# Kernel tuning notes

Measured on AMD Instinct MI355X. Metric: run time of the kernel, lower is better.

Reference implementation:

```python
import jax, jax.numpy as jnp
import numpy as np

D_MODEL = 512
NUM_HEADS = 8
HEAD_DIM = D_MODEL // NUM_HEADS
EPS = 1e-6


def setup_inputs() -> dict:
    key = jax.random.key(0)
    ks = jax.random.split(key, 9)
    s = 1.0 / np.sqrt(D_MODEL)
    x = jax.random.normal(ks[0], (4, 8192, D_MODEL), dtype=jnp.float32)
    Wq = jax.random.uniform(ks[1], (D_MODEL, D_MODEL), jnp.float32, -s, s)
    bq = jax.random.uniform(ks[2], (D_MODEL,), jnp.float32, -s, s)
    Wk = jax.random.uniform(ks[3], (D_MODEL, D_MODEL), jnp.float32, -s, s)
    bk = jax.random.uniform(ks[4], (D_MODEL,), jnp.float32, -s, s)
    Wv = jax.random.uniform(ks[5], (D_MODEL, D_MODEL), jnp.float32, -s, s)
    bv = jax.random.uniform(ks[6], (D_MODEL,), jnp.float32, -s, s)
    Wo = jax.random.uniform(ks[7], (D_MODEL, D_MODEL), jnp.float32, -s, s)
    bo = jax.random.uniform(ks[8], (D_MODEL,), jnp.float32, -s, s)
    return {"x": x, "Wq": Wq, "bq": bq, "Wk": Wk, "bk": bk,
            "Wv": Wv, "bv": bv, "Wo": Wo, "bo": bo}


def _feature_map(t):
    # ELU(x) + 1
    return jax.nn.elu(t) + 1.0


def reference(x, Wq, bq, Wk, bk, Wv, bv, Wo, bo):
    B, N, C = x.shape
    H, D = NUM_HEADS, HEAD_DIM
    # projections: torch Linear computes x @ W.T + b
    q = (x @ Wq.T + bq).reshape(B, N, H, D).transpose(0, 2, 1, 3)  # [B,H,N,D]
    k = (x @ Wk.T + bk).reshape(B, N, H, D).transpose(0, 2, 1, 3)
    v = (x @ Wv.T + bv).reshape(B, N, H, D).transpose(0, 2, 1, 3)
    q = _feature_map(q)
    k = _feature_map(k)
    # kv: [B,H,D,D] = k^T v   (global, non-causal linear attention)
    kv = jnp.einsum('bhnd,bhne->bhde', k, v)
    # normalizer: q . sum_n(k)  -> [B,H,N,1]
    k_sum = k.sum(axis=2)  # [B,H,D]
    z = jnp.einsum('bhnd,bhd->bhn', q, k_sum)[..., None] + EPS
    out = jnp.einsum('bhnd,bhde->bhne', q, kv) / z  # [B,H,N,D]
    out = out.transpose(0, 2, 1, 3).reshape(B, N, C)
    return out @ Wo.T + bo
```

## Files before the change

kernel.cpp:

```cpp
#include <hip/hip_runtime.h>
#include <hip/hip_bf16.h>

typedef __attribute__((ext_vector_type(8))) short short8;
typedef __attribute__((ext_vector_type(4))) float f32x4;
typedef unsigned short u16;
typedef unsigned int u32;

#define T_TOK 32768
#define CDIM  512
#define HEADS 8
#define HD    64
#define NSEQ  8192

#define AS1 __attribute__((address_space(1)))
#define AS3 __attribute__((address_space(3)))

__device__ __forceinline__ u16 f2bf(float f) {
  u32 u = __builtin_bit_cast(u32, f);
  u = u + 0x7fffu + ((u >> 16) & 1u);
  return (u16)(u >> 16);
}
__device__ __forceinline__ float bf2f(u16 s) {
  return __builtin_bit_cast(float, ((u32)s) << 16);
}

__global__ __launch_bounds__(256) void k_convx(const float* __restrict__ x,
                                               u16* __restrict__ xb) {
  size_t i = (size_t)blockIdx.x * 256 + threadIdx.x;
  size_t stride = (size_t)gridDim.x * 256;
  size_t total = (size_t)T_TOK * 512 / 8;
  for (; i < total; i += stride) {
    float4 a = *reinterpret_cast<const float4*>(&x[i * 8]);
    float4 b = *reinterpret_cast<const float4*>(&x[i * 8 + 4]);
    ushort4 r0, r1;
    r0.x = f2bf(a.x); r0.y = f2bf(a.y); r0.z = f2bf(a.z); r0.w = f2bf(a.w);
    r1.x = f2bf(b.x); r1.y = f2bf(b.y); r1.z = f2bf(b.z); r1.w = f2bf(b.w);
    *reinterpret_cast<ushort4*>(&xb[i * 8])     = r0;
    *reinterpret_cast<ushort4*>(&xb[i * 8 + 4]) = r1;
  }
}

__global__ void k_pack_w(const float* __restrict__ Wq, const float* __restrict__ Wk,
                         const float* __restrict__ Wv, const float* __restrict__ Wo,
                         u16* __restrict__ Wcat) {
  int idx = blockIdx.x * 256 + threadIdx.x;
  int c = idx & 511;
  int o2 = idx >> 9;
  const float* W = (o2 < 512) ? Wq : (o2 < 1024) ? Wk : (o2 < 1536) ? Wv : Wo;
  int o = o2 & 511;
  Wcat[idx] = f2bf(W[o * 512 + c]);
}

__global__ __launch_bounds__(256, 2) void k_gemm0(const u16* __restrict__ Ag,
    const u16* __restrict__ Wcat,
    const float* __restrict__ b0, const float* __restrict__ b1, const float* __restrict__ b2,
    u16* __restrict__ qkv) {
  constexpr int NT = 6;
  __shared__ u16 As[128][64];
  __shared__ u16 Bs[256][64];
  int bid = blockIdx.x;
  constexpr int GRID = (T_TOK / 128) * NT;
  constexpr int CHUNK = GRID / 8;
  int swz = (bid & 7) * CHUNK + (bid >> 3);
  int m0 = (swz / NT) * 128;
  int n0 = (swz % NT) * 256;
  int tid = threadIdx.x;
  int lane = tid & 63, w = tid >> 6;
  int wr = w >> 1, wc = w & 1;
  f32x4 acc_a[4][4], acc_b[4][4];
  _Pragma("unroll")
  for (int i = 0; i < 4; ++i)
    _Pragma("unroll")
    for (int j = 0; j < 4; ++j) { acc_a[i][j] = (f32x4)0.0f; acc_b[i][j] = (f32x4)0.0f; }

  int grl = lane >> 3;
  int gcl = (((lane & 7) ^ grl)) * 8;
  int l15 = lane & 15, lhi = lane >> 4, sx = lane & 7;

  for (int t = 0; t < 8; ++t) {
    int k0 = t * 64;
    _Pragma("unroll")
    for (int i = 0; i < 4; ++i) {
      int r = w * 32 + i * 8;
      __builtin_amdgcn_global_load_lds(
          (const AS1 void*)&Ag[(size_t)(m0 + r + grl) * 512 + k0 + gcl],
          (AS3 void*)&As[r][0], 16, 0, 0);
    }
    _Pragma("unroll")
    for (int i = 0; i < 8; ++i) {
      int r = w * 64 + i * 8;
      __builtin_amdgcn_global_load_lds(
          (const AS1 void*)&Wcat[(size_t)(n0 + r + grl) * 512 + k0 + gcl],
          (AS3 void*)&Bs[r][0], 16, 0, 0);
    }
    __syncthreads();
    _Pragma("unroll")
    for (int kk = 0; kk < 2; ++kk) {
      int slot = (kk * 4 + lhi) ^ sx;
      short8 af[4], bfa[4], bfb[4];
      _Pragma("unroll")
      for (int m = 0; m < 4; ++m)
        af[m] = *reinterpret_cast<const short8*>(&As[wr * 64 + m * 16 + l15][slot * 8]);
      _Pragma("unroll")
      for (int n = 0; n < 4; ++n)
        bfa[n] = *reinterpret_cast<const short8*>(&Bs[wc * 128 + n * 16 + l15][slot * 8]);
      _Pragma("unroll")
      for (int n = 0; n < 4; ++n)
        bfb[n] = *reinterpret_cast<const short8*>(&Bs[wc * 128 + 64 + n * 16 + l15][slot * 8]);
      _Pragma("unroll")
      for (int m = 0; m < 4; ++m)
        _Pragma("unroll")
        for (int n = 0; n < 4; ++n)
          acc_a[m][n] = __builtin_amdgcn_mfma_f32_16x16x32_bf16(af[m], bfa[n], acc_a[m][n], 0, 0, 0);
      _Pragma("unroll")
      for (int m = 0; m < 4; ++m)
        _Pragma("unroll")
        for (int n = 0; n < 4; ++n)
          acc_b[m][n] = __builtin_amdgcn_mfma_f32_16x16x32_bf16(af[m], bfb[n], acc_b[m][n], 0, 0, 0);
    }
    __syncthreads();
  }

  _Pragma("unroll")
  for (int m = 0; m < 4; ++m) {
    int row = m0 + wr * 64 + m * 16 + lhi * 4;
    _Pragma("unroll")
    for (int nh = 0; nh < 2; ++nh) {
      _Pragma("unroll")
      for (int n = 0; n < 4; ++n) {
        int col = n0 + wc * 128 + nh * 64 + n * 16 + l15;
        float bias = (col < 512) ? b0[col] : (col < 1024) ? b1[col - 512] : b2[col - 1024];
        _Pragma("unroll")
        for (int j = 0; j < 4; ++j) {
          float vv = (nh == 0 ? acc_a[m][n][j] : acc_b[m][n][j]) + bias;
          if (col < 1024) vv = (vv > 0.0f) ? (vv + 1.0f) : __expf(vv);
          qkv[(size_t)(row + j) * 1536 + col] = f2bf(vv);
        }
      }
    }
  }
}

__global__ __launch_bounds__(256, 4) void k_gemm1(const u16* __restrict__ Ag,
    const u16* __restrict__ Wcat, const float* __restrict__ b0,
    float* __restrict__ out) {
  constexpr int NT = 4;
  __shared__ u16 As[128][64];
  __shared__ u16 Bs[128][64];
  int bid = blockIdx.x;
  constexpr int GRID = (T_TOK / 128) * NT;
  constexpr int CHUNK = GRID / 8;
  int swz = (bid & 7) * CHUNK + (bid >> 3);
  int m0 = (swz / NT) * 128;
  int n0 = (swz % NT) * 128;
  int tid = threadIdx.x;
  int lane = tid & 63, w = tid >> 6;
  int wr = w >> 1, wc = w & 1;
  f32x4 acc[4][4];
  _Pragma("unroll")
  for (int i = 0; i < 4; ++i)
    _Pragma("unroll")
    for (int j = 0; j < 4; ++j) acc[i][j] = (f32x4)0.0f;

  const u16* Bg = Wcat + (size_t)1536 * 512;
  int grl = lane >> 3;
  int gcl = (((lane & 7) ^ grl)) * 8;
  int l15 = lane & 15, lhi = lane >> 4, sx = lane & 7;

  for (int t = 0; t < 8; ++t) {
    int k0 = t * 64;
    _Pragma("unroll")
    for (int i = 0; i < 4; ++i) {
      int r = w * 32 + i * 8;
      __builtin_amdgcn_global_load_lds(
          (const AS1 void*)&Ag[(size_t)(m0 + r + grl) * 512 + k0 + gcl],
          (AS3 void*)&As[r][0], 16, 0, 0);
      __builtin_amdgcn_global_load_lds(
          (const AS1 void*)&Bg[(size_t)(n0 + r + grl) * 512 + k0 + gcl],
          (AS3 void*)&Bs[r][0], 16, 0, 0);
    }
    __syncthreads();
    _Pragma("unroll")
    for (int kk = 0; kk < 2; ++kk) {
      int slot = (kk * 4 + lhi) ^ sx;
      short8 af[4], bfr[4];
      _Pragma("unroll")
      for (int m = 0; m < 4; ++m)
        af[m] = *reinterpret_cast<const short8*>(&As[wr * 64 + m * 16 + l15][slot * 8]);
      _Pragma("unroll")
      for (int n = 0; n < 4; ++n)
        bfr[n] = *reinterpret_cast<const short8*>(&Bs[wc * 64 + n * 16 + l15][slot * 8]);
      _Pragma("unroll")
      for (int m = 0; m < 4; ++m)
        _Pragma("unroll")
        for (int n = 0; n < 4; ++n)
          acc[m][n] = __builtin_amdgcn_mfma_f32_16x16x32_bf16(af[m], bfr[n], acc[m][n], 0, 0, 0);
    }
    __syncthreads();
  }

  _Pragma("unroll")
  for (int m = 0; m < 4; ++m) {
    int row = m0 + wr * 64 + m * 16 + lhi * 4;
    _Pragma("unroll")
    for (int n = 0; n < 4; ++n) {
      int col = n0 + wc * 64 + n * 16 + l15;
      float bias = b0[col];
      _Pragma("unroll")
      for (int j = 0; j < 4; ++j)
        out[(size_t)(row + j) * 512 + col] = acc[m][n][j] + bias;
    }
  }
}

__global__ __launch_bounds__(256) void k_kvstats(const u16* __restrict__ qkv,
    float* __restrict__ kvp, float* __restrict__ ksp) {
  __shared__ u16 kt[64][32];
  __shared__ u16 vt[64][32];
  __shared__ float ks_red[4][64];
  int hh = blockIdx.x;
  int s  = blockIdx.y;
  int b = hh >> 3, h = hh & 7;
  int tid = threadIdx.x;
  int lane = tid & 63, w = tid >> 6;
  size_t tbase = (size_t)b * NSEQ + (size_t)s * 512;
  f32x4 acc[4];
  for (int n = 0; n < 4; ++n) acc[n] = (f32x4)0.0f;
  float ksum_loc = 0.0f;
  int kcol = 512 + h * 64;
  int vcol = 1024 + h * 64;
  int l15 = lane & 15;
  int rsw = 8 * (l15 >> 2);

  for (int step = 0; step < 16; ++step) {
    size_t t0 = tbase + (size_t)step * 32;
    for (int jj = 0; jj < 4; ++jj) {
      int id = tid + 256 * jj;
      int trow = (id >> 4) & 31;
      int dq = id & 15;
      int isv = id >> 9;
      ushort4 val = *reinterpret_cast<const ushort4*>(
          &qkv[(t0 + trow) * 1536 + (isv ? vcol : kcol) + dq * 4]);
      u16 (*dst)[32] = isv ? vt : kt;
      int colw = trow ^ (8 * (dq & 3));
      dst[dq * 4 + 0][colw] = val.x;
      dst[dq * 4 + 1][colw] = val.y;
      dst[dq * 4 + 2][colw] = val.z;
      dst[dq * 4 + 3][colw] = val.w;
    }
    __syncthreads();
    {
      int d = tid & 63, g = tid >> 6;
      int gs = 8 * (g ^ ((d >> 2) & 3));
      float sl = 0;
      for (int i = 0; i < 8; ++i) sl += bf2f(kt[d][gs + i]);
      ksum_loc += sl;
    }
    int kb = 8 * (lane >> 4);
    short8 af = *reinterpret_cast<const short8*>(&kt[w * 16 + l15][kb ^ rsw]);
    for (int n = 0; n < 4; ++n) {
      short8 bfr = *reinterpret_cast<const short8*>(&vt[n * 16 + l15][kb ^ rsw]);
      acc[n] = __builtin_amdgcn_mfma_f32_16x16x32_bf16(af, bfr, acc[n], 0, 0, 0);
    }
    __syncthreads();
  }
  size_t pbase = ((size_t)hh * 16 + s) * 4096;
  for (int n = 0; n < 4; ++n) {
    int d = w * 16 + (lane >> 4) * 4;
    int e = n * 16 + (lane & 15);
    for (int j = 0; j < 4; ++j)
      kvp[pbase + (size_t)(d + j) * 64 + e] = acc[n][j];
  }
  ks_red[tid >> 6][tid & 63] = ksum_loc;
  __syncthreads();
  if (tid < 64) {
    float r = ks_red[0][tid] + ks_red[1][tid] + ks_red[2][tid] + ks_red[3][tid];
    ksp[((size_t)hh * 16 + s) * 64 + tid] = r;
  }
}

__global__ void k_reduce(const float* __restrict__ kvp, const float* __restrict__ ksp,
                         u16* __restrict__ kvb, float* __restrict__ ksum) {
  int hh = blockIdx.x;
  int sl = blockIdx.y;
  int tid = threadIdx.x;
  for (int j = 0; j < 2; ++j) {
    int idx = sl * 512 + tid + 256 * j;
    float a = 0;
    for (int s = 0; s < 16; ++s) a += kvp[((size_t)hh * 16 + s) * 4096 + idx];
    int d = idx >> 6, e = idx & 63;
    kvb[(size_t)hh * 4096 + e * 64 + d] = f2bf(a);
  }
  if (sl == 0 && tid < 64) {
    float a = 0;
    for (int s = 0; s < 16; ++s) a += ksp[((size_t)hh * 16 + s) * 64 + tid];
    ksum[hh * 64 + tid] = a;
  }
}

__global__ __launch_bounds__(256) void k_attn(const u16* __restrict__ qkv,
    const u16* __restrict__ kvb, const float* __restrict__ ksum,
    u16* __restrict__ attn) {
  __shared__ u16 qf[32][520];
  __shared__ float zl[32][8];
  __shared__ float kss[8][64];
  int tid = threadIdx.x;
  int lane = tid & 63, w = tid >> 6;
  size_t t0 = (size_t)blockIdx.x * 32;
  int b = (int)(t0 >> 13);
  for (int jj = 0; jj < 16; ++jj) {
    int id = tid + 256 * jj;
    int row = id >> 7, cq = id & 127;
    *reinterpret_cast<ushort4*>(&qf[row][cq * 4]) =
        *reinterpret_cast<const ushort4*>(&qkv[(t0 + row) * 1536 + cq * 4]);
  }
  { int i = tid, i2 = tid + 256;
    kss[i >> 6][i & 63]   = ksum[b * 512 + i];
    kss[i2 >> 6][i2 & 63] = ksum[b * 512 + i2]; }
  __syncthreads();
  {
    int tok = tid & 31, h = tid >> 5;
    float z = 0;
    for (int jq = 0; jq < 8; ++jq) {
      short8 qv = *reinterpret_cast<const short8*>(&qf[tok][h * 64 + jq * 8]);
      for (int e = 0; e < 8; ++e) z += bf2f((u16)qv[e]) * kss[h][jq * 8 + e];
    }
    zl[tok][h] = z + 1e-6f;
  }
  __syncthreads();
  for (int hi = 0; hi < 2; ++hi) {
    int h = w * 2 + hi;
    size_t kvoff = (size_t)(b * 8 + h) * 4096;
    f32x4 acc[2][4];
    for (int m = 0; m < 2; ++m) for (int n = 0; n < 4; ++n) acc[m][n] = (f32x4)0.0f;
    for (int kk = 0; kk < 2; ++kk) {
      int kb = kk * 32 + 8 * (lane >> 4);
      short8 af[2], bfr[4];
      for (int m = 0; m < 2; ++m)
        af[m] = *reinterpret_cast<const short8*>(&qf[m * 16 + (lane & 15)][h * 64 + kb]);
      for (int n = 0; n < 4; ++n)
        bfr[n] = *reinterpret_cast<const short8*>(&kvb[kvoff + (size_t)(n * 16 + (lane & 15)) * 64 + kb]);
      for (int m = 0; m < 2; ++m)
        for (int n = 0; n < 4; ++n)
          acc[m][n] = __builtin_amdgcn_mfma_f32_16x16x32_bf16(af[m], bfr[n], acc[m][n], 0, 0, 0);
    }
    for (int m = 0; m < 2; ++m) {
      int tokb = m * 16 + (lane >> 4) * 4;
      for (int n = 0; n < 4; ++n) {
        int e = n * 16 + (lane & 15);
        for (int j = 0; j < 4; ++j) {
          float vv = acc[m][n][j] / zl[tokb + j][h];
          attn[(t0 + tokb + j) * 512 + h * 64 + e] = f2bf(vv);
        }
      }
    }
  }
}

extern "C" void kernel_launch(void* const* d_in, const int* in_sizes, int n_in,
                              void* d_out, int out_size, void* d_ws, size_t ws_size,
                              hipStream_t stream) {
  const float* x  = (const float*)d_in[0];
  const float* Wq = (const float*)d_in[1];
  const float* bq = (const float*)d_in[2];
  const float* Wk = (const float*)d_in[3];
  const float* bk = (const float*)d_in[4];
  const float* Wv = (const float*)d_in[5];
  const float* bv = (const float*)d_in[6];
  const float* Wo = (const float*)d_in[7];
  const float* bo = (const float*)d_in[8];
  float* out = (float*)d_out;

  char* ws = (char*)d_ws;
  u16*   Wcat = (u16*)(ws + 0);
  u16*   qkv  = (u16*)(ws + 2097152);
  u16*   xb   = (u16*)(ws + 102760448);
  float* kvp  = (float*)(ws + 102760448);
  u16*   attn = (u16*)(ws + 102760448);
  float* ksp  = (float*)(ws + 136314880);
  u16*   kvb  = (u16*)(ws + 136445952);
  float* ksum = (float*)(ws + 136708096);

  k_convx  <<<2048, 256, 0, stream>>>(x, xb);
  k_pack_w <<<4096, 256, 0, stream>>>(Wq, Wk, Wv, Wo, Wcat);
  k_gemm0  <<<1536, 256, 0, stream>>>(xb, Wcat, bq, bk, bv, qkv);
  k_kvstats<<<dim3(32, 16), 256, 0, stream>>>(qkv, kvp, ksp);
  k_reduce <<<dim3(32, 8), 256, 0, stream>>>(kvp, ksp, kvb, ksum);
  k_attn   <<<1024, 256, 0, stream>>>(qkv, kvb, ksum, attn);
  k_gemm1  <<<1024, 256, 0, stream>>>(attn, Wcat, bo, out);
}
```

Before: 170.3 us.

## Fuse fp32-to-bf16 conversion of x into QKV GEMM A-tile loads

Removes the separate x conversion kernel and has the QKV projection GEMM read fp32 x directly, converting to bf16 in registers before writing swizzled LDS tiles. To keep registers low, the N tile is halved from 256 to 128 (12 column tiles, 3072 blocks), with occupancy raised to 4 blocks per CU. This saves a 64MB write plus a 32MB read of the bf16 copy, but each x tile is now reloaded as fp32 by 12 blocks instead of 6, and the A path uses synchronous register loads instead of direct-to-LDS async loads.

```diff
diff --git a/kernel.cpp b/kernel.cpp
--- a/kernel.cpp
+++ b/kernel.cpp
@@ -22,22 +22,6 @@
 }
 __device__ __forceinline__ float bf2f(u16 s) {
   return __builtin_bit_cast(float, ((u32)s) << 16);
-}
-
-__global__ __launch_bounds__(256) void k_convx(const float* __restrict__ x,
-                                               u16* __restrict__ xb) {
-  size_t i = (size_t)blockIdx.x * 256 + threadIdx.x;
-  size_t stride = (size_t)gridDim.x * 256;
-  size_t total = (size_t)T_TOK * 512 / 8;
-  for (; i < total; i += stride) {
-    float4 a = *reinterpret_cast<const float4*>(&x[i * 8]);
-    float4 b = *reinterpret_cast<const float4*>(&x[i * 8 + 4]);
-    ushort4 r0, r1;
-    r0.x = f2bf(a.x); r0.y = f2bf(a.y); r0.z = f2bf(a.z); r0.w = f2bf(a.w);
-    r1.x = f2bf(b.x); r1.y = f2bf(b.y); r1.z = f2bf(b.z); r1.w = f2bf(b.w);
-    *reinterpret_cast<ushort4*>(&xb[i * 8])     = r0;
-    *reinterpret_cast<ushort4*>(&xb[i * 8 + 4]) = r1;
-  }
 }
 
 __global__ void k_pack_w(const float* __restrict__ Wq, const float* __restrict__ Wk,
@@ -51,72 +35,74 @@
   Wcat[idx] = f2bf(W[o * 512 + c]);
 }
 
-__global__ __launch_bounds__(256, 2) void k_gemm0(const u16* __restrict__ Ag,
+__global__ __launch_bounds__(256, 4) void k_gemm0(const float* __restrict__ x,
     const u16* __restrict__ Wcat,
     const float* __restrict__ b0, const float* __restrict__ b1, const float* __restrict__ b2,
     u16* __restrict__ qkv) {
-  constexpr int NT = 6;
+  constexpr int NT = 12;
   __shared__ u16 As[128][64];
-  __shared__ u16 Bs[256][64];
+  __shared__ u16 Bs[128][64];
   int bid = blockIdx.x;
   constexpr int GRID = (T_TOK / 128) * NT;
   constexpr int CHUNK = GRID / 8;
   int swz = (bid & 7) * CHUNK + (bid >> 3);
   int m0 = (swz / NT) * 128;
-  int n0 = (swz % NT) * 256;
+  int n0 = (swz % NT) * 128;
   int tid = threadIdx.x;
   int lane = tid & 63, w = tid >> 6;
   int wr = w >> 1, wc = w & 1;
-  f32x4 acc_a[4][4], acc_b[4][4];
+  f32x4 acc[4][4];
   _Pragma("unroll")
   for (int i = 0; i < 4; ++i)
     _Pragma("unroll")
-    for (int j = 0; j < 4; ++j) { acc_a[i][j] = (f32x4)0.0f; acc_b[i][j] = (f32x4)0.0f; }
+    for (int j = 0; j < 4; ++j) acc[i][j] = (f32x4)0.0f;
 
   int grl = lane >> 3;
   int gcl = (((lane & 7) ^ grl)) * 8;
   int l15 = lane & 15, lhi = lane >> 4, sx = lane & 7;
 
+  int arow = tid >> 1;
+  int ac0  = (tid & 1) * 32;
+  int sl0  = (tid & 1) * 4;
+  int asw  = arow & 7;
+  const float* xrow = &x[(size_t)(m0 + arow) * 512];
+
   for (int t = 0; t < 8; ++t) {
     int k0 = t * 64;
     _Pragma("unroll")
     for (int i = 0; i < 4; ++i) {
       int r = w * 32 + i * 8;
       __builtin_amdgcn_global_load_lds(
-          (const AS1 void*)&Ag[(size_t)(m0 + r + grl) * 512 + k0 + gcl],
-          (AS3 void*)&As[r][0], 16, 0, 0);
-    }
-    _Pragma("unroll")
-    for (int i = 0; i < 8; ++i) {
-      int r = w * 64 + i * 8;
-      __builtin_amdgcn_global_load_lds(
           (const AS1 void*)&Wcat[(size_t)(n0 + r + grl) * 512 + k0 + gcl],
           (AS3 void*)&Bs[r][0], 16, 0, 0);
     }
+    _Pragma("unroll")
+    for (int j = 0; j < 4; ++j) {
+      float4 lo = *reinterpret_cast<const float4*>(&xrow[k0 + ac0 + j * 8]);
+      float4 hi = *reinterpret_cast<const float4*>(&xrow[k0 + ac0 + j * 8 + 4]);
+      short8 p;
+      p[0] = (short)f2bf(lo.x); p[1] = (short)f2bf(lo.y);
+      p[2] = (short)f2bf(lo.z); p[3] = (short)f2bf(lo.w);
+      p[4] = (short)f2bf(hi.x); p[5] = (short)f2bf(hi.y);
+      p[6] = (short)f2bf(hi.z); p[7] = (short)f2bf(hi.w);
+      *reinterpret_cast<short8*>(&As[arow][((sl0 + j) ^ asw) * 8]) = p;
+    }
     __syncthreads();
     _Pragma("unroll")
     for (int kk = 0; kk < 2; ++kk) {
       int slot = (kk * 4 + lhi) ^ sx;
-      short8 af[4], bfa[4], bfb[4];
+      short8 af[4], bfr[4];
       _Pragma("unroll")
       for (int m = 0; m < 4; ++m)
         af[m] = *reinterpret_cast<const short8*>(&As[wr * 64 + m * 16 + l15][slot * 8]);
       _Pragma("unroll")
       for (int n = 0; n < 4; ++n)
-        bfa[n] = *reinterpret_cast<const short8*>(&Bs[wc * 128 + n * 16 + l15][slot * 8]);
-      _Pragma("unroll")
-      for (int n = 0; n < 4; ++n)
-        bfb[n] = *reinterpret_cast<const short8*>(&Bs[wc * 128 + 64 + n * 16 + l15][slot * 8]);
+        bfr[n] = *reinterpret_cast<const short8*>(&Bs[wc * 64 + n * 16 + l15][slot * 8]);
       _Pragma("unroll")
       for (int m = 0; m < 4; ++m)
         _Pragma("unroll")
         for (int n = 0; n < 4; ++n)
-          acc_a[m][n] = __builtin_amdgcn_mfma_f32_16x16x32_bf16(af[m], bfa[n], acc_a[m][n], 0, 0, 0);
-      _Pragma("unroll")
-      for (int m = 0; m < 4; ++m)
-        _Pragma("unroll")
-        for (int n = 0; n < 4; ++n)
-          acc_b[m][n] = __builtin_amdgcn_mfma_f32_16x16x32_bf16(af[m], bfb[n], acc_b[m][n], 0, 0, 0);
+          acc[m][n] = __builtin_amdgcn_mfma_f32_16x16x32_bf16(af[m], bfr[n], acc[m][n], 0, 0, 0);
     }
     __syncthreads();
   }
@@ -125,17 +111,14 @@
   for (int m = 0; m < 4; ++m) {
     int row = m0 + wr * 64 + m * 16 + lhi * 4;
     _Pragma("unroll")
-    for (int nh = 0; nh < 2; ++nh) {
-      _Pragma("unroll")
-      for (int n = 0; n < 4; ++n) {
-        int col = n0 + wc * 128 + nh * 64 + n * 16 + l15;
-        float bias = (col < 512) ? b0[col] : (col < 1024) ? b1[col - 512] : b2[col - 1024];
-        _Pragma("unroll")
-        for (int j = 0; j < 4; ++j) {
-          float vv = (nh == 0 ? acc_a[m][n][j] : acc_b[m][n][j]) + bias;
-          if (col < 1024) vv = (vv > 0.0f) ? (vv + 1.0f) : __expf(vv);
-          qkv[(size_t)(row + j) * 1536 + col] = f2bf(vv);
-        }
+    for (int n = 0; n < 4; ++n) {
+      int col = n0 + wc * 64 + n * 16 + l15;
+      float bias = (col < 512) ? b0[col] : (col < 1024) ? b1[col - 512] : b2[col - 1024];
+      _Pragma("unroll")
+      for (int j = 0; j < 4; ++j) {
+        float vv = acc[m][n][j] + bias;
+        if (col < 1024) vv = (vv > 0.0f) ? (vv + 1.0f) : __expf(vv);
+        qkv[(size_t)(row + j) * 1536 + col] = f2bf(vv);
       }
     }
   }
@@ -374,16 +357,14 @@
   char* ws = (char*)d_ws;
   u16*   Wcat = (u16*)(ws + 0);
   u16*   qkv  = (u16*)(ws + 2097152);
-  u16*   xb   = (u16*)(ws + 102760448);
   float* kvp  = (float*)(ws + 102760448);
   u16*   attn = (u16*)(ws + 102760448);
   float* ksp  = (float*)(ws + 136314880);
   u16*   kvb  = (u16*)(ws + 136445952);
   float* ksum = (float*)(ws + 136708096);
 
-  k_convx  <<<2048, 256, 0, stream>>>(x, xb);
   k_pack_w <<<4096, 256, 0, stream>>>(Wq, Wk, Wv, Wo, Wcat);
-  k_gemm0  <<<1536, 256, 0, stream>>>(xb, Wcat, bq, bk, bv, qkv);
+  k_gemm0  <<<3072, 256, 0, stream>>>(x, Wcat, bq, bk, bv, qkv);
   k_kvstats<<<dim3(32, 16), 256, 0, stream>>>(qkv, kvp, ksp);
   k_reduce <<<dim3(32, 8), 256, 0, stream>>>(kvp, ksp, kvb, ksum);
   k_attn   <<<1024, 256, 0, stream>>>(qkv, kvb, ksum, attn);
```

Measured after the change: 230.3 us. 35.3% more time.
